# Kernel optimization log

Hardware: AMD Instinct MI355X
Metric: run time of the kernel (lower is better)

## Reference

```python
import jax, jax.numpy as jnp
import numpy as np

K, D = 1024, 256
B, H, W = 16, 64, 64


def setup_inputs() -> dict:
    key = jax.random.key(0)
    k1, k2 = jax.random.split(key)
    z_e_x = jax.random.normal(k1, (B, D, H, W), dtype=jnp.float32)
    # nn.Embedding weight initialized uniform(-1/K, 1/K)
    embedding = jax.random.uniform(k2, (K, D), dtype=jnp.float32,
                                   minval=-1.0 / K, maxval=1.0 / K)
    return {"z_e_x": z_e_x, "embedding": embedding}


def reference(z_e_x, embedding):
    # permute(0,2,3,1): [B,D,H,W] -> [B,H,W,D]
    z = jnp.transpose(z_e_x, (0, 2, 3, 1))
    flat = z.reshape(-1, z.shape[-1])  # [N, D], N = B*H*W
    # squared L2 distances: ||z||^2 - 2 z.e + ||e||^2  -> [N, K]
    dists = (jnp.sum(flat * flat, axis=1, keepdims=True)
             - 2.0 * flat @ embedding.T
             + jnp.sum(embedding * embedding, axis=1))
    indices = jnp.argmin(dists, axis=1)  # [N]
    # vq() returns latents with the spatial shape [B, H, W]
    return indices.reshape(z.shape[:-1]).astype(jnp.int32)
```

## Files before the change

kernel.cpp:

```cpp
#include <hip/hip_runtime.h>


#define D_DIM 256
#define K_DIM 1024
#define HW    4096
#define N_TOT 65536
#define BN    128
#define BK    128
#define DC    32
#define LDP   132


__global__ void ee_kernel(const float* __restrict__ e, float* __restrict__ ee) {
#pragma clang fp contract(off)
    int k = blockIdx.x * blockDim.x + threadIdx.x;
    if (k >= K_DIM) return;
    const float* row = e + (size_t)k * D_DIM;
    float total = 0.0f;
    #pragma unroll
    for (int h = 0; h < 2; ++h) {
        const float* a = row + h * 128;
        float r[8];
        #pragma unroll
        for (int j = 0; j < 8; ++j) { float v = a[j]; r[j] = v * v; }
        #pragma unroll
        for (int i = 8; i < 128; i += 8) {
            #pragma unroll
            for (int j = 0; j < 8; ++j) { float v = a[i + j]; r[j] = r[j] + v * v; }
        }
        float s = ((r[0] + r[1]) + (r[2] + r[3])) + ((r[4] + r[5]) + (r[6] + r[7]));
        total = (h == 0) ? s : (total + s);
    }
    ee[k] = total;
}

__global__ void a_kernel(const float* __restrict__ z, float* __restrict__ A) {
#pragma clang fp contract(off)
    int n = blockIdx.x * blockDim.x + threadIdx.x;
    int b  = n >> 12;
    int hw = n & (HW - 1);
    const float* base = z + (size_t)b * D_DIM * HW + hw;
    float total = 0.0f;
    #pragma unroll
    for (int h = 0; h < 2; ++h) {
        float r[8];
        #pragma unroll
        for (int j = 0; j < 8; ++j) {
            float v = base[(size_t)(h * 128 + j) * HW];
            r[j] = v * v;
        }
        #pragma unroll
        for (int i = 8; i < 128; i += 8) {
            #pragma unroll
            for (int j = 0; j < 8; ++j) {
                float v = base[(size_t)(h * 128 + i + j) * HW];
                r[j] = r[j] + v * v;
            }
        }
        float s = ((r[0] + r[1]) + (r[2] + r[3])) + ((r[4] + r[5]) + (r[6] + r[7]));
        total = (h == 0) ? s : (total + s);
    }
    A[n] = total;
}


__launch_bounds__(256)
__global__ void vq_kernel(const float* __restrict__ z, const float* __restrict__ emb,
                          const float* __restrict__ A, const float* __restrict__ ee,
                          int* __restrict__ out) {
#pragma clang fp contract(off)
    __shared__ __align__(16) float zs[DC * LDP];
    __shared__ __align__(16) float es[DC * LDP];

    const int tid = threadIdx.x;
    const int tx = tid & 15;
    const int ty = tid >> 4;
    const int n0 = blockIdx.x * BN;
    const int b   = n0 >> 12;
    const int hw0 = n0 & (HW - 1);
    const float* zbase = z + (size_t)b * D_DIM * HW + hw0;

    float bestv[8];
    int   bestk[8];
    #pragma unroll
    for (int i = 0; i < 8; ++i) { bestv[i] = 3.402823466e38f; bestk[i] = 0; }

    for (int kt = 0; kt < K_DIM / BK; ++kt) {
        float acc[8][8];
        #pragma unroll
        for (int i = 0; i < 8; ++i)
            #pragma unroll
            for (int j = 0; j < 8; ++j) acc[i][j] = 0.0f;

        for (int c = 0; c < D_DIM / DC; ++c) {
            const int d0 = c * DC;
            __syncthreads();
            #pragma unroll
            for (int q = 0; q < 4; ++q) {
                int fidx = tid + 256 * q;
                int dl = fidx >> 5, n4 = (fidx & 31) * 4;
                float4 v = *(const float4*)(zbase + (size_t)(d0 + dl) * HW + n4);
                float4 w;
                w.x = 2.0f * v.x; w.y = 2.0f * v.y; w.z = 2.0f * v.z; w.w = 2.0f * v.w;
                *(float4*)&zs[dl * LDP + n4] = w;
            }
            #pragma unroll
            for (int r = 0; r < 4; ++r) {
                int kl = (tid >> 3) + 32 * r;
                int dq = tid & 7;
                float4 v = *(const float4*)(emb + (size_t)(kt * BK + kl) * D_DIM + d0 + dq * 4);
                es[(dq * 4 + 0) * LDP + kl] = v.x;
                es[(dq * 4 + 1) * LDP + kl] = v.y;
                es[(dq * 4 + 2) * LDP + kl] = v.z;
                es[(dq * 4 + 3) * LDP + kl] = v.w;
            }
            __syncthreads();
            #pragma unroll 4
            for (int dd = 0; dd < DC; ++dd) {
                float4 z0 = *(const float4*)&zs[dd * LDP + 4 * ty];
                float4 z1 = *(const float4*)&zs[dd * LDP + 64 + 4 * ty];
                float4 e0 = *(const float4*)&es[dd * LDP + 4 * tx];
                float4 e1 = *(const float4*)&es[dd * LDP + 64 + 4 * tx];
                float zr[8] = {z0.x, z0.y, z0.z, z0.w, z1.x, z1.y, z1.z, z1.w};
                float er[8] = {e0.x, e0.y, e0.z, e0.w, e1.x, e1.y, e1.z, e1.w};
                #pragma unroll
                for (int i = 0; i < 8; ++i)
                    #pragma unroll
                    for (int j = 0; j < 8; ++j)
                        acc[i][j] = fmaf(zr[i], er[j], acc[i][j]);
            }
        }
        #pragma unroll
        for (int i = 0; i < 8; ++i) {
            int nl = (i < 4) ? (4 * ty + i) : (64 + 4 * ty + (i - 4));
            float An = A[n0 + nl];
            #pragma unroll
            for (int j = 0; j < 8; ++j) {
                int kg = kt * BK + ((j < 4) ? (4 * tx + j) : (64 + 4 * tx + (j - 4)));
                float t1 = An - acc[i][j];
                float dist = t1 + ee[kg];
                if (dist < bestv[i]) { bestv[i] = dist; bestk[i] = kg; }
            }
        }
    }
    #pragma unroll
    for (int i = 0; i < 8; ++i) {
        float v = bestv[i];
        int   kk = bestk[i];
        #pragma unroll
        for (int off = 8; off >= 1; off >>= 1) {
            float ov = __shfl_xor(v, off, 64);
            int   ok = __shfl_xor(kk, off, 64);
            if (ov < v || (ov == v && ok < kk)) { v = ov; kk = ok; }
        }
        if (tx == 0) {
            int nl = (i < 4) ? (4 * ty + i) : (64 + 4 * ty + (i - 4));
            out[n0 + nl] = kk;
        }
    }
}

extern "C" void kernel_launch(void* const* d_in, const int* in_sizes, int n_in,
                              void* d_out, int out_size, void* d_ws, size_t ws_size,
                              hipStream_t stream) {
    const float* z   = (const float*)d_in[0];
    const float* emb = (const float*)d_in[1];
    int* out = (int*)d_out;

    float* wsA  = (float*)d_ws;
    float* wsEE = wsA + N_TOT;

    ee_kernel<<<K_DIM / 256, 256, 0, stream>>>(emb, wsEE);
    a_kernel<<<N_TOT / 256, 256, 0, stream>>>(z, wsA);
    vq_kernel<<<N_TOT / BN, 256, 0, stream>>>(z, emb, wsA, wsEE, out);
}
```

Baseline: 532.8 us.

## Double-buffer shared tiles with register prefetch and widen per-thread K tile

Restructures the VQ distance kernel into a single flattened loop over (K-tile, D-chunk) stages. The next stage's global loads are prefetched into registers and written into the alternate shared-memory buffer while the current one is consumed, leaving one barrier per stage. The K tile doubles to 256, so each thread accumulates an 8x16 block and reuses each z value across more codebook entries, and the A values are hoisted out of the loop. This raises register pressure (128 accumulators plus prefetch registers under a 2-waves launch bound), which risks spills or lower occupancy.

```diff
diff --git a/kernel.cpp b/kernel.cpp
--- a/kernel.cpp
+++ b/kernel.cpp
@@ -6,9 +6,9 @@
 #define HW    4096
 #define N_TOT 65536
 #define BN    128
-#define BK    128
-#define DC    32
-#define LDP   132
+#define BK    256
+#define DC    16
+#define LDE   260
 
 
 __global__ void ee_kernel(const float* __restrict__ e, float* __restrict__ ee) {
@@ -64,13 +64,13 @@
 }
 
 
-__launch_bounds__(256)
+__launch_bounds__(256, 2)
 __global__ void vq_kernel(const float* __restrict__ z, const float* __restrict__ emb,
                           const float* __restrict__ A, const float* __restrict__ ee,
                           int* __restrict__ out) {
 #pragma clang fp contract(off)
-    __shared__ __align__(16) float zs[DC * LDP];
-    __shared__ __align__(16) float es[DC * LDP];
+    __shared__ __align__(16) float zs[2][DC * BN];
+    __shared__ __align__(16) float es[2][DC * LDE];
 
     const int tid = threadIdx.x;
     const int tx = tid & 15;
@@ -80,69 +80,123 @@
     const int hw0 = n0 & (HW - 1);
     const float* zbase = z + (size_t)b * D_DIM * HW + hw0;
 
-    float bestv[8];
-    int   bestk[8];
+    const int zdl0 = tid >> 5, zn0 = (tid & 31) * 4;
+    const int zdl1 = (tid + 256) >> 5, zn1 = zn0;
+    const int edq4 = (tid & 3) * 4;
+    const int ekb  = tid >> 2;
+
+    float An[8];
+    #pragma unroll
+    for (int i = 0; i < 8; ++i) An[i] = A[n0 + 4 * ty + (i & 3) + 64 * (i >> 2)];
+
+    float bestv[8]; int bestk[8];
     #pragma unroll
     for (int i = 0; i < 8; ++i) { bestv[i] = 3.402823466e38f; bestk[i] = 0; }
 
-    for (int kt = 0; kt < K_DIM / BK; ++kt) {
-        float acc[8][8];
-        #pragma unroll
-        for (int i = 0; i < 8; ++i)
-            #pragma unroll
-            for (int j = 0; j < 8; ++j) acc[i][j] = 0.0f;
-
-        for (int c = 0; c < D_DIM / DC; ++c) {
-            const int d0 = c * DC;
-            __syncthreads();
-            #pragma unroll
-            for (int q = 0; q < 4; ++q) {
-                int fidx = tid + 256 * q;
-                int dl = fidx >> 5, n4 = (fidx & 31) * 4;
-                float4 v = *(const float4*)(zbase + (size_t)(d0 + dl) * HW + n4);
-                float4 w;
-                w.x = 2.0f * v.x; w.y = 2.0f * v.y; w.z = 2.0f * v.z; w.w = 2.0f * v.w;
-                *(float4*)&zs[dl * LDP + n4] = w;
+    float acc[8][16];
+    #pragma unroll
+    for (int i = 0; i < 8; ++i)
+        #pragma unroll
+        for (int j = 0; j < 16; ++j) acc[i][j] = 0.0f;
+
+    float4 zp0, zp1, ep0, ep1, ep2, ep3;
+
+    {
+        const int d0 = 0, k0 = 0;
+        zp0 = *(const float4*)(zbase + (size_t)(d0 + zdl0) * HW + zn0);
+        zp1 = *(const float4*)(zbase + (size_t)(d0 + zdl1) * HW + zn1);
+        const float* eb = emb + (size_t)(k0 + ekb) * D_DIM + d0 + edq4;
+        ep0 = *(const float4*)(eb);
+        ep1 = *(const float4*)(eb + 64 * D_DIM);
+        ep2 = *(const float4*)(eb + 128 * D_DIM);
+        ep3 = *(const float4*)(eb + 192 * D_DIM);
+    }
+    {
+        float4 w0, w1;
+        w0.x = 2.0f*zp0.x; w0.y = 2.0f*zp0.y; w0.z = 2.0f*zp0.z; w0.w = 2.0f*zp0.w;
+        w1.x = 2.0f*zp1.x; w1.y = 2.0f*zp1.y; w1.z = 2.0f*zp1.z; w1.w = 2.0f*zp1.w;
+        *(float4*)&zs[0][zdl0 * BN + zn0] = w0;
+        *(float4*)&zs[0][zdl1 * BN + zn1] = w1;
+        float* e0p = &es[0][edq4 * LDE + ekb];
+        e0p[0*LDE +   0] = ep0.x; e0p[1*LDE +   0] = ep0.y; e0p[2*LDE +   0] = ep0.z; e0p[3*LDE +   0] = ep0.w;
+        e0p[0*LDE +  64] = ep1.x; e0p[1*LDE +  64] = ep1.y; e0p[2*LDE +  64] = ep1.z; e0p[3*LDE +  64] = ep1.w;
+        e0p[0*LDE + 128] = ep2.x; e0p[1*LDE + 128] = ep2.y; e0p[2*LDE + 128] = ep2.z; e0p[3*LDE + 128] = ep2.w;
+        e0p[0*LDE + 192] = ep3.x; e0p[1*LDE + 192] = ep3.y; e0p[2*LDE + 192] = ep3.z; e0p[3*LDE + 192] = ep3.w;
+    }
+
+    for (int s = 0; s < 64; ++s) {
+        const int cur = s & 1;
+
+        if (s < 63) {
+            const int sn = s + 1;
+            const int d0 = (sn & 15) * DC;
+            const int k0 = (sn >> 4) * BK;
+            zp0 = *(const float4*)(zbase + (size_t)(d0 + zdl0) * HW + zn0);
+            zp1 = *(const float4*)(zbase + (size_t)(d0 + zdl1) * HW + zn1);
+            const float* eb = emb + (size_t)(k0 + ekb) * D_DIM + d0 + edq4;
+            ep0 = *(const float4*)(eb);
+            ep1 = *(const float4*)(eb + 64 * D_DIM);
+            ep2 = *(const float4*)(eb + 128 * D_DIM);
+            ep3 = *(const float4*)(eb + 192 * D_DIM);
+        }
+
+        __syncthreads();
+
+        #pragma unroll 4
+        for (int dd = 0; dd < DC; ++dd) {
+            const float* zr0p = &zs[cur][dd * BN + 4 * ty];
+            float4 z0 = *(const float4*)zr0p;
+            float4 z1 = *(const float4*)(zr0p + 64);
+            const float* erp = &es[cur][dd * LDE + 4 * tx];
+            float4 e0 = *(const float4*)(erp);
+            float4 e1 = *(const float4*)(erp + 64);
+            float4 e2 = *(const float4*)(erp + 128);
+            float4 e3 = *(const float4*)(erp + 192);
+            float zr[8]  = {z0.x, z0.y, z0.z, z0.w, z1.x, z1.y, z1.z, z1.w};
+            float er[16] = {e0.x, e0.y, e0.z, e0.w, e1.x, e1.y, e1.z, e1.w,
+                            e2.x, e2.y, e2.z, e2.w, e3.x, e3.y, e3.z, e3.w};
+            #pragma unroll
+            for (int i = 0; i < 8; ++i)
+                #pragma unroll
+                for (int j = 0; j < 16; ++j)
+                    acc[i][j] = fmaf(zr[i], er[j], acc[i][j]);
+        }
+
+        if (s < 63) {
+            const int nxt = cur ^ 1;
+            float4 w0, w1;
+            w0.x = 2.0f*zp0.x; w0.y = 2.0f*zp0.y; w0.z = 2.0f*zp0.z; w0.w = 2.0f*zp0.w;
+            w1.x = 2.0f*zp1.x; w1.y = 2.0f*zp1.y; w1.z = 2.0f*zp1.z; w1.w = 2.0f*zp1.w;
+            *(float4*)&zs[nxt][zdl0 * BN + zn0] = w0;
+            *(float4*)&zs[nxt][zdl1 * BN + zn1] = w1;
+            float* e0p = &es[nxt][edq4 * LDE + ekb];
+            e0p[0*LDE +   0] = ep0.x; e0p[1*LDE +   0] = ep0.y; e0p[2*LDE +   0] = ep0.z; e0p[3*LDE +   0] = ep0.w;
+            e0p[0*LDE +  64] = ep1.x; e0p[1*LDE +  64] = ep1.y; e0p[2*LDE +  64] = ep1.z; e0p[3*LDE +  64] = ep1.w;
+            e0p[0*LDE + 128] = ep2.x; e0p[1*LDE + 128] = ep2.y; e0p[2*LDE + 128] = ep2.z; e0p[3*LDE + 128] = ep2.w;
+            e0p[0*LDE + 192] = ep3.x; e0p[1*LDE + 192] = ep3.y; e0p[2*LDE + 192] = ep3.z; e0p[3*LDE + 192] = ep3.w;
+        }
+
+        if ((s & 15) == 15) {
+            const int kt = s >> 4;
+            float eev[16];
+            #pragma unroll
+            for (int j = 0; j < 16; ++j)
+                eev[j] = ee[kt * BK + 4 * tx + (j & 3) + 64 * (j >> 2)];
+            #pragma unroll
+            for (int i = 0; i < 8; ++i) {
+                const float a = An[i];
+                #pragma unroll
+                for (int j = 0; j < 16; ++j) {
+                    const int kg = kt * BK + 4 * tx + (j & 3) + 64 * (j >> 2);
+                    const float t1 = a - acc[i][j];
+                    const float dist = t1 + eev[j];
+                    if (dist < bestv[i]) { bestv[i] = dist; bestk[i] = kg; }
+                    acc[i][j] = 0.0f;
+                }
             }
-            #pragma unroll
-            for (int r = 0; r < 4; ++r) {
-                int kl = (tid >> 3) + 32 * r;
-                int dq = tid & 7;
-                float4 v = *(const float4*)(emb + (size_t)(kt * BK + kl) * D_DIM + d0 + dq * 4);
-                es[(dq * 4 + 0) * LDP + kl] = v.x;
-                es[(dq * 4 + 1) * LDP + kl] = v.y;
-                es[(dq * 4 + 2) * LDP + kl] = v.z;
-                es[(dq * 4 + 3) * LDP + kl] = v.w;
-            }
-            __syncthreads();
-            #pragma unroll 4
-            for (int dd = 0; dd < DC; ++dd) {
-                float4 z0 = *(const float4*)&zs[dd * LDP + 4 * ty];
-                float4 z1 = *(const float4*)&zs[dd * LDP + 64 + 4 * ty];
-                float4 e0 = *(const float4*)&es[dd * LDP + 4 * tx];
-                float4 e1 = *(const float4*)&es[dd * LDP + 64 + 4 * tx];
-                float zr[8] = {z0.x, z0.y, z0.z, z0.w, z1.x, z1.y, z1.z, z1.w};
-                float er[8] = {e0.x, e0.y, e0.z, e0.w, e1.x, e1.y, e1.z, e1.w};
-                #pragma unroll
-                for (int i = 0; i < 8; ++i)
-                    #pragma unroll
-                    for (int j = 0; j < 8; ++j)
-                        acc[i][j] = fmaf(zr[i], er[j], acc[i][j]);
-            }
-        }
-        #pragma unroll
-        for (int i = 0; i < 8; ++i) {
-            int nl = (i < 4) ? (4 * ty + i) : (64 + 4 * ty + (i - 4));
-            float An = A[n0 + nl];
-            #pragma unroll
-            for (int j = 0; j < 8; ++j) {
-                int kg = kt * BK + ((j < 4) ? (4 * tx + j) : (64 + 4 * tx + (j - 4)));
-                float t1 = An - acc[i][j];
-                float dist = t1 + ee[kg];
-                if (dist < bestv[i]) { bestv[i] = dist; bestk[i] = kg; }
-            }
-        }
-    }
+        }
+    }
+
     #pragma unroll
     for (int i = 0; i < 8; ++i) {
         float v = bestv[i];
@@ -153,10 +207,7 @@
             int   ok = __shfl_xor(kk, off, 64);
             if (ov < v || (ov == v && ok < kk)) { v = ov; kk = ok; }
         }
-        if (tx == 0) {
-            int nl = (i < 4) ? (4 * ty + i) : (64 + 4 * ty + (i - 4));
-            out[n0 + nl] = kk;
-        }
+        if (tx == 0) out[n0 + 4 * ty + (i & 3) + 64 * (i >> 2)] = kk;
     }
 }
 
```

Result: faster. 522.0 us (-2.0%).

## Restructure VQ argmin as per-thread rows with split-K partials and combine

Applied to the files above, without the earlier changes.

The LDS-tiled 8x8 register-blocked GEMM is replaced by a scheme with one query row per thread. Each thread keeps 64 accumulators and streams a pre-transposed, pre-doubled codebook whose addresses are uniform across the wavefront, so the loads can become broadcast or scalar loads and no LDS or barriers are needed. The codebook dimension is split four ways across blocks to add parallelism, and a new combine kernel reduces the partial minima. The cost is re-reading z from global memory for every K tile and split, plus extra transpose and combine launches and workspace traffic.

```diff
diff --git a/kernel.cpp b/kernel.cpp
--- a/kernel.cpp
+++ b/kernel.cpp
@@ -1,14 +1,15 @@
 #include <hip/hip_runtime.h>
 
 
-#define D_DIM 256
-#define K_DIM 1024
-#define HW    4096
-#define N_TOT 65536
-#define BN    128
-#define BK    128
-#define DC    32
-#define LDP   132
+#define D_DIM  256
+#define K_DIM  1024
+#define HW     4096
+#define N_TOT  65536
+#define NSPLIT 4
+#define KSPL   (K_DIM / NSPLIT)
+#define KT     64
+#define NKT    (KSPL / KT)
+#define F32MAX 3.402823466e38f
 
 
 __global__ void ee_kernel(const float* __restrict__ e, float* __restrict__ ee) {
@@ -64,100 +65,93 @@
 }
 
 
-__launch_bounds__(256)
-__global__ void vq_kernel(const float* __restrict__ z, const float* __restrict__ emb,
-                          const float* __restrict__ A, const float* __restrict__ ee,
-                          int* __restrict__ out) {
+__global__ void et_kernel(const float* __restrict__ e, float* __restrict__ eT) {
+    int k = blockIdx.x;
+    int d = threadIdx.x;
+    eT[(size_t)d * K_DIM + k] = 2.0f * e[(size_t)k * D_DIM + d];
+}
+
+
+__launch_bounds__(256, 4)
+__global__ void vq_partial(const float* __restrict__ z, const float* __restrict__ eT,
+                           const float* __restrict__ A, const float* __restrict__ ee,
+                           float* __restrict__ pv, int* __restrict__ pk) {
 #pragma clang fp contract(off)
-    __shared__ __align__(16) float zs[DC * LDP];
-    __shared__ __align__(16) float es[DC * LDP];
+    const int tid  = threadIdx.x;
+    const int s    = blockIdx.x & (NSPLIT - 1);
+    const int slab = blockIdx.x >> 2;
+    const int n    = slab * 256 + tid;
+    const int b    = n >> 12;
+    const int hw   = n & (HW - 1);
+    const float* __restrict__ zp = z + (size_t)b * D_DIM * HW + hw;
+    const int kb0 = s * KSPL;
 
-    const int tid = threadIdx.x;
-    const int tx = tid & 15;
-    const int ty = tid >> 4;
-    const int n0 = blockIdx.x * BN;
-    const int b   = n0 >> 12;
-    const int hw0 = n0 & (HW - 1);
-    const float* zbase = z + (size_t)b * D_DIM * HW + hw0;
+    const float An = A[n];
+    float bestv = F32MAX;
+    int   bestk = 0;
 
-    float bestv[8];
-    int   bestk[8];
+    float za[8], zb[8];
     #pragma unroll
-    for (int i = 0; i < 8; ++i) { bestv[i] = 3.402823466e38f; bestk[i] = 0; }
+    for (int i = 0; i < 8; ++i) za[i] = zp[(size_t)i * HW];
 
-    for (int kt = 0; kt < K_DIM / BK; ++kt) {
-        float acc[8][8];
+    #pragma unroll 1
+    for (int kt = 0; kt < NKT; ++kt) {
+        const int kbase = kb0 + kt * KT;
+        float acc[KT];
         #pragma unroll
-        for (int i = 0; i < 8; ++i)
+        for (int j = 0; j < KT; ++j) acc[j] = 0.0f;
+
+        #pragma unroll 1
+        for (int it = 0; it < 16; ++it) {
+            const int base = it * 16;
             #pragma unroll
-            for (int j = 0; j < 8; ++j) acc[i][j] = 0.0f;
-
-        for (int c = 0; c < D_DIM / DC; ++c) {
-            const int d0 = c * DC;
-            __syncthreads();
+            for (int i = 0; i < 8; ++i)
+                zb[i] = zp[(size_t)((base + 8 + i) & (D_DIM - 1)) * HW];
             #pragma unroll
-            for (int q = 0; q < 4; ++q) {
-                int fidx = tid + 256 * q;
-                int dl = fidx >> 5, n4 = (fidx & 31) * 4;
-                float4 v = *(const float4*)(zbase + (size_t)(d0 + dl) * HW + n4);
-                float4 w;
-                w.x = 2.0f * v.x; w.y = 2.0f * v.y; w.z = 2.0f * v.z; w.w = 2.0f * v.w;
-                *(float4*)&zs[dl * LDP + n4] = w;
+            for (int dd = 0; dd < 8; ++dd) {
+                const float zv = za[dd];
+                const float* __restrict__ er = eT + (size_t)(base + dd) * K_DIM + kbase;
+                #pragma unroll
+                for (int j = 0; j < KT; ++j)
+                    acc[j] = fmaf(zv, er[j], acc[j]);
             }
             #pragma unroll
-            for (int r = 0; r < 4; ++r) {
-                int kl = (tid >> 3) + 32 * r;
-                int dq = tid & 7;
-                float4 v = *(const float4*)(emb + (size_t)(kt * BK + kl) * D_DIM + d0 + dq * 4);
-                es[(dq * 4 + 0) * LDP + kl] = v.x;
-                es[(dq * 4 + 1) * LDP + kl] = v.y;
-                es[(dq * 4 + 2) * LDP + kl] = v.z;
-                es[(dq * 4 + 3) * LDP + kl] = v.w;
-            }
-            __syncthreads();
-            #pragma unroll 4
-            for (int dd = 0; dd < DC; ++dd) {
-                float4 z0 = *(const float4*)&zs[dd * LDP + 4 * ty];
-                float4 z1 = *(const float4*)&zs[dd * LDP + 64 + 4 * ty];
-                float4 e0 = *(const float4*)&es[dd * LDP + 4 * tx];
-                float4 e1 = *(const float4*)&es[dd * LDP + 64 + 4 * tx];
-                float zr[8] = {z0.x, z0.y, z0.z, z0.w, z1.x, z1.y, z1.z, z1.w};
-                float er[8] = {e0.x, e0.y, e0.z, e0.w, e1.x, e1.y, e1.z, e1.w};
+            for (int i = 0; i < 8; ++i)
+                za[i] = zp[(size_t)((base + 16 + i) & (D_DIM - 1)) * HW];
+            #pragma unroll
+            for (int dd = 0; dd < 8; ++dd) {
+                const float zv = zb[dd];
+                const float* __restrict__ er = eT + (size_t)(base + 8 + dd) * K_DIM + kbase;
                 #pragma unroll
-                for (int i = 0; i < 8; ++i)
-                    #pragma unroll
-                    for (int j = 0; j < 8; ++j)
-                        acc[i][j] = fmaf(zr[i], er[j], acc[i][j]);
+                for (int j = 0; j < KT; ++j)
+                    acc[j] = fmaf(zv, er[j], acc[j]);
             }
         }
+
         #pragma unroll
-        for (int i = 0; i < 8; ++i) {
-            int nl = (i < 4) ? (4 * ty + i) : (64 + 4 * ty + (i - 4));
-            float An = A[n0 + nl];
-            #pragma unroll
-            for (int j = 0; j < 8; ++j) {
-                int kg = kt * BK + ((j < 4) ? (4 * tx + j) : (64 + 4 * tx + (j - 4)));
-                float t1 = An - acc[i][j];
-                float dist = t1 + ee[kg];
-                if (dist < bestv[i]) { bestv[i] = dist; bestk[i] = kg; }
-            }
+        for (int j = 0; j < KT; ++j) {
+            const float dist = (An - acc[j]) + ee[kbase + j];
+            if (dist < bestv) { bestv = dist; bestk = kbase + j; }
         }
     }
+
+    pv[(size_t)s * N_TOT + n] = bestv;
+    pk[(size_t)s * N_TOT + n] = bestk;
+}
+
+
+__global__ void combine_kernel(const float* __restrict__ pv, const int* __restrict__ pk,
+                               int* __restrict__ out) {
+    int n = blockIdx.x * blockDim.x + threadIdx.x;
+    float bv = pv[n];
+    int   bk = pk[n];
     #pragma unroll
-    for (int i = 0; i < 8; ++i) {
-        float v = bestv[i];
-        int   kk = bestk[i];
-        #pragma unroll
-        for (int off = 8; off >= 1; off >>= 1) {
-            float ov = __shfl_xor(v, off, 64);
-            int   ok = __shfl_xor(kk, off, 64);
-            if (ov < v || (ov == v && ok < kk)) { v = ov; kk = ok; }
-        }
-        if (tx == 0) {
-            int nl = (i < 4) ? (4 * ty + i) : (64 + 4 * ty + (i - 4));
-            out[n0 + nl] = kk;
-        }
+    for (int s2 = 1; s2 < NSPLIT; ++s2) {
+        float v = pv[(size_t)s2 * N_TOT + n];
+        int   k = pk[(size_t)s2 * N_TOT + n];
+        if (v < bv) { bv = v; bk = k; }
     }
+    out[n] = bk;
 }
 
 extern "C" void kernel_launch(void* const* d_in, const int* in_sizes, int n_in,
@@ -169,8 +163,13 @@
 
     float* wsA  = (float*)d_ws;
     float* wsEE = wsA + N_TOT;
+    float* wsET = wsEE + K_DIM;
+    float* wsPV = wsET + (size_t)D_DIM * K_DIM;
+    int*   wsPK = (int*)(wsPV + (size_t)NSPLIT * N_TOT);
 
+    et_kernel<<<K_DIM, 256, 0, stream>>>(emb, wsET);
     ee_kernel<<<K_DIM / 256, 256, 0, stream>>>(emb, wsEE);
     a_kernel<<<N_TOT / 256, 256, 0, stream>>>(z, wsA);
-    vq_kernel<<<N_TOT / BN, 256, 0, stream>>>(z, emb, wsA, wsEE, out);
+    vq_partial<<<N_TOT / 256 * NSPLIT, 256, 0, stream>>>(z, wsET, wsA, wsEE, wsPV, wsPK);
+    combine_kernel<<<N_TOT / 256, 256, 0, stream>>>(wsPV, wsPK, out);
 }
```

Result: faster. 511.9 us (-3.9%).
